# Kernel tuning notes

Measured on AMD Instinct MI355X. Metric: run time of the kernel, lower is better.

Reference implementation:

```python
import jax, jax.numpy as jnp
import numpy as np

B, C, H, W = 256, 1024, 14, 14
C8 = C // 8
TXT = 150 * 1024  # flattened text embed dim
N = H * W  # 196, matches self.l shape (1,196)


def setup_inputs() -> dict:
    key = jax.random.key(0)
    ks = jax.random.split(key, 12)
    s = lambda fan_in: 1.0 / np.sqrt(fan_in)
    return {
        "x": jax.random.normal(ks[0], (B, C, H, W), jnp.float32),
        "text_embed": jax.random.normal(ks[1], (B, 1, 150, 1024), jnp.float32),
        "G_w": jax.random.normal(ks[2], (C, TXT), jnp.float32) * s(TXT),
        "G_b": jnp.zeros((C,), jnp.float32),
        "l": jax.random.normal(ks[3], (1, N), jnp.float32) * 0.02,
        "W_q": jax.random.normal(ks[4], (C8, C), jnp.float32) * s(C),
        "b_q": jnp.zeros((C8,), jnp.float32),
        "W_k": jax.random.normal(ks[5], (C8, C), jnp.float32) * s(C),
        "b_k": jnp.zeros((C8,), jnp.float32),
        "W_v": jax.random.normal(ks[6], (C, C), jnp.float32) * s(C),
        "b_v": jnp.zeros((C,), jnp.float32),
        "gamma": jnp.ones((1,), jnp.float32) * 0.5,
    }


def reference(x, text_embed, G_w, G_b, l, W_q, b_q, W_k, b_k, W_v, b_v, gamma):
    b, c, h, w = x.shape
    n = h * w
    # text preprocessing: squeeze(1) + flatten + Linear G -> (B, C)
    te = text_embed.reshape(b, -1) @ G_w.T + G_b  # (B, C)
    # bmm(te[:, :, None], l broadcast) == outer product per batch -> (B, C, N)
    te_flat = te[:, :, None] * l[None, 0, None, :]  # (B, C, N)
    x_flat = x.reshape(b, c, n)  # (B, C, N)
    # 1x1 convs == channel matmuls
    proj_query = jnp.einsum('qc,bcn->bnq', W_q, x_flat) + b_q  # (B, N, C8)
    proj_key = jnp.einsum('kc,bcn->bkn', W_k, te_flat) + b_k[None, :, None]  # (B, C8, N)
    energy = jnp.einsum('bnq,bqm->bnm', proj_query, proj_key)  # (B, N, N)
    attention = jax.nn.softmax(energy, axis=-1)  # (B, N, N)
    proj_value = jnp.einsum('vc,bcn->bvn', W_v, te_flat) + b_v[None, :, None]  # (B, C, N)
    # out = bmm(value, attention^T): out[b,c,m] = sum_n value[b,c,n] * attn[b,m,n]
    out = jnp.einsum('bcn,bmn->bcm', proj_value, attention)  # (B, C, N)
    out = out.reshape(b, c, h, w)
    return gamma * out + x
```

## Files before the change

kernel.cpp:

```cpp
#include <hip/hip_runtime.h>
#include <hip/hip_bf16.h>

#define BB 256
#define CC 1024
#define CQ 128
#define NN 196
#define TXTK 153600
#define SPLITS 64
#define KCHUNK 2400
#define KSTEPS 75
#define LDP 40

typedef __attribute__((ext_vector_type(8))) short short8;
typedef __attribute__((ext_vector_type(4))) float f32x4;
typedef __attribute__((ext_vector_type(2))) unsigned int u32x2;

static __device__ __forceinline__ unsigned int pkbf(float a, float b) {
  __hip_bfloat162 t = __float22bfloat162_rn(make_float2(a, b));
  unsigned int r;
  __builtin_memcpy(&r, &t, 4);
  return r;
}

static __device__ __forceinline__ float bflo(unsigned int u) {
  unsigned int v = u << 16;
  float f;
  __builtin_memcpy(&f, &v, 4);
  return f;
}
static __device__ __forceinline__ float bfhi(unsigned int u) {
  unsigned int v = u & 0xffff0000u;
  float f;
  __builtin_memcpy(&f, &v, 4);
  return f;
}

__global__ __launch_bounds__(1024) void k1_gemm_partial(
    const float* __restrict__ TE, const float* __restrict__ Gw,
    unsigned int* __restrict__ part) {
  __shared__ unsigned short Al[2][256 * LDP];
  __shared__ unsigned short Bl[2][256 * LDP];

  const int tid = threadIdx.x;
  const int fid = blockIdx.x;
  const int r8 = fid & 7;
  const int nt = (fid >> 3) & 3;
  const int sp = (fid >> 5) * 8 + r8;
  const int kbase = sp * KCHUNK;

  const int lane = tid & 63;
  const int w = tid >> 6;
  const int wm = w & 3;
  const int wn = w >> 2;

  const int r0 = tid >> 3;
  const int c0 = (tid & 7) * 4;
  const float* Ap0 = TE + (size_t)r0 * TXTK + kbase + c0;
  const float* Ap1 = TE + (size_t)(r0 + 128) * TXTK + kbase + c0;
  const float* Bp0 = Gw + (size_t)(nt * 256 + r0) * TXTK + kbase + c0;
  const float* Bp1 = Gw + (size_t)(nt * 256 + r0 + 128) * TXTK + kbase + c0;
  const int l0 = r0 * LDP + c0;
  const int l1 = (r0 + 128) * LDP + c0;

  f32x4 ra0, ra1, rb0, rb1;
  auto loadRegs = [&](int ko) {
    ra0 = *(const f32x4*)(Ap0 + ko);
    ra1 = *(const f32x4*)(Ap1 + ko);
    rb0 = __builtin_nontemporal_load((const f32x4*)(Bp0 + ko));
    rb1 = __builtin_nontemporal_load((const f32x4*)(Bp1 + ko));
  };
  auto cvt4 = [](f32x4 v) {
    uint2 h;
    h.x = pkbf(v.x, v.y);
    h.y = pkbf(v.z, v.w);
    return h;
  };
  auto writeLDS = [&](int buf) {
    *(uint2*)&Al[buf][l0] = cvt4(ra0);
    *(uint2*)&Al[buf][l1] = cvt4(ra1);
    *(uint2*)&Bl[buf][l0] = cvt4(rb0);
    *(uint2*)&Bl[buf][l1] = cvt4(rb1);
  };

  f32x4 acc[4][4];
  const f32x4 z = {0.f, 0.f, 0.f, 0.f};
#pragma unroll
  for (int i = 0; i < 4; ++i)
#pragma unroll
    for (int j = 0; j < 4; ++j) acc[i][j] = z;

  loadRegs(0);
  writeLDS(0);
  __syncthreads();

  const int k8 = (lane >> 4) * 8;
  const int fr = lane & 15;

  for (int ks = 0; ks < KSTEPS; ++ks) {
    const int cur = ks & 1;
    if (ks + 1 < KSTEPS) loadRegs((ks + 1) * 32);

    short8 bfr[4];
#pragma unroll
    for (int ns = 0; ns < 4; ++ns) {
      int col = wn * 64 + ns * 16 + fr;
      bfr[ns] = *(const short8*)&Bl[cur][col * LDP + k8];
    }
#pragma unroll
    for (int ms = 0; ms < 4; ++ms) {
      int row = wm * 64 + ms * 16 + fr;
      short8 af = *(const short8*)&Al[cur][row * LDP + k8];
#pragma unroll
      for (int ns = 0; ns < 4; ++ns)
        acc[ms][ns] = __builtin_amdgcn_mfma_f32_16x16x32_bf16(af, bfr[ns], acc[ms][ns], 0, 0, 0);
    }

    if (ks + 1 < KSTEPS) writeLDS(cur ^ 1);
    __syncthreads();
  }

  u32x2* d2 = (u32x2*)part + (size_t)(sp * 4 + nt) * 16384;
#pragma unroll
  for (int ms = 0; ms < 4; ++ms)
#pragma unroll
    for (int ns = 0; ns < 4; ++ns) {
      u32x2 pk;
      pk.x = pkbf(acc[ms][ns][0], acc[ms][ns][1]);
      pk.y = pkbf(acc[ms][ns][2], acc[ms][ns][3]);
      const int v = ms * 4 + ns;
      __builtin_nontemporal_store(pk, d2 + v * 1024 + tid);
    }
}

__global__ __launch_bounds__(1024) void k2_reduce(
    const unsigned int* __restrict__ part, const float* __restrict__ Gb,
    float* __restrict__ te) {
  const int idx = blockIdx.x * 1024 + threadIdx.x;
  const int nt = idx >> 14;
  const int s = idx & 16383;
  const u32x2* p2 = (const u32x2*)part;

  float a0 = 0.f, a1 = 0.f, a2 = 0.f, a3 = 0.f;
#pragma unroll 4
  for (int sp = 0; sp < SPLITS; ++sp) {
    u32x2 u = p2[(size_t)(sp * 4 + nt) * 16384 + s];
    a0 += bflo(u.x); a1 += bfhi(u.x);
    a2 += bflo(u.y); a3 += bfhi(u.y);
  }

  const int v = s >> 10, t = s & 1023;
  const int lane = t & 63, w = t >> 6;
  const int wm = w & 3, wn = w >> 2;
  const int ms = v >> 2, ns = v & 3;
  const int b0 = wm * 64 + ms * 16 + (lane >> 4) * 4;
  const int c = nt * 256 + wn * 64 + ns * 16 + (lane & 15);
  const float gb = Gb[c];
  te[(size_t)(b0 + 0) * CC + c] = a0 + gb;
  te[(size_t)(b0 + 1) * CC + c] = a1 + gb;
  te[(size_t)(b0 + 2) * CC + c] = a2 + gb;
  te[(size_t)(b0 + 3) * CC + c] = a3 + gb;
}

__global__ __launch_bounds__(256) void k3_dual(
    const float* __restrict__ te, const float* __restrict__ Wk,
    const float* __restrict__ Wv, float* __restrict__ kbuf,
    float* __restrict__ vbuf) {
  __shared__ float As[64][33];
  __shared__ float Bs[64][33];
  const int tid = threadIdx.x;
  const int tx = tid & 15, ty = tid >> 4;
  const int bx = blockIdx.x;
  const float* Wt;
  float* outp;
  int Nout, n0;
  if (bx < 2) { Wt = Wk; outp = kbuf; Nout = CQ; n0 = bx * 64; }
  else        { Wt = Wv; outp = vbuf; Nout = CC; n0 = (bx - 2) * 64; }
  const int m0 = blockIdx.y * 64;
  float acc[4][4] = {};
  for (int k0 = 0; k0 < CC; k0 += 32) {
#pragma unroll
    for (int j = 0; j < 2; ++j) {
      int i = tid + 256 * j;
      int r = i >> 3, c4 = (i & 7) * 4;
      f32x4 va = *(const f32x4*)(te + (size_t)(m0 + r) * CC + k0 + c4);
      As[r][c4 + 0] = va.x; As[r][c4 + 1] = va.y; As[r][c4 + 2] = va.z; As[r][c4 + 3] = va.w;
      f32x4 vb4 = *(const f32x4*)(Wt + (size_t)(n0 + r) * CC + k0 + c4);
      Bs[r][c4 + 0] = vb4.x; Bs[r][c4 + 1] = vb4.y; Bs[r][c4 + 2] = vb4.z; Bs[r][c4 + 3] = vb4.w;
    }
    __syncthreads();
#pragma unroll 8
    for (int k = 0; k < 32; ++k) {
      float a[4], bv[4];
#pragma unroll
      for (int i = 0; i < 4; ++i) a[i] = As[ty * 4 + i][k];
#pragma unroll
      for (int j = 0; j < 4; ++j) bv[j] = Bs[tx * 4 + j][k];
#pragma unroll
      for (int i = 0; i < 4; ++i)
#pragma unroll
        for (int j = 0; j < 4; ++j) acc[i][j] += a[i] * bv[j];
    }
    __syncthreads();
  }
#pragma unroll
  for (int i = 0; i < 4; ++i)
#pragma unroll
    for (int j = 0; j < 4; ++j)
      outp[(size_t)(m0 + ty * 4 + i) * Nout + n0 + tx * 4 + j] = acc[i][j];
}

__global__ __launch_bounds__(1024) void k4a_attn(
    const float* __restrict__ x, const float* __restrict__ kb,
    const float* __restrict__ Wq, const float* __restrict__ bq,
    float* __restrict__ pbuf) {
  __shared__ float kbs[CQ];
  __shared__ float wqs[512];
  __shared__ float partl[16][NN];
  __shared__ float dsh;

  const int h = blockIdx.x;
  const int b = blockIdx.y;
  const int ch0 = h * 512;
  const int tid = threadIdx.x;

  if (tid < CQ) kbs[tid] = kb[b * CQ + tid];
  __syncthreads();

  if (tid < 512) {
    float s = 0.f;
#pragma unroll 8
    for (int q = 0; q < CQ; ++q) s += Wq[q * CC + ch0 + tid] * kbs[q];
    wqs[tid] = s;
  }
  if (tid == 1023) {
    float d = 0.f;
    if (h == 0)
      for (int q = 0; q < CQ; ++q) d += bq[q] * kbs[q];
    dsh = d;
  }
  __syncthreads();

  const float* xb = x + (size_t)b * (CC * NN) + (size_t)ch0 * NN;
  if (tid < 784) {
    const int r = tid / 49, n4 = tid % 49;
    f32x4 acc = {0.f, 0.f, 0.f, 0.f};
#pragma unroll 4
    for (int c = r; c < 512; c += 16) {
      f32x4 v = *(const f32x4*)(xb + c * NN + n4 * 4);
      acc += wqs[c] * v;
    }
    partl[r][n4 * 4 + 0] = acc.x;
    partl[r][n4 * 4 + 1] = acc.y;
    partl[r][n4 * 4 + 2] = acc.z;
    partl[r][n4 * 4 + 3] = acc.w;
  }
  __syncthreads();
  if (tid < NN) {
    float s = dsh;
#pragma unroll
    for (int r = 0; r < 16; ++r) s += partl[r][tid];
    pbuf[b * 400 + h * 200 + tid] = s;
  }
}

__global__ __launch_bounds__(256) void k4mid(
    const float* __restrict__ pbuf, const float* __restrict__ l,
    float* __restrict__ sbuf) {
  __shared__ float ls[NN];
  __shared__ float av[NN];
  const int b = blockIdx.x;
  const int tid = threadIdx.x;
  if (tid < NN) {
    ls[tid] = l[tid];
    av[tid] = pbuf[b * 400 + tid] + pbuf[b * 400 + 200 + tid];
  }
  __syncthreads();
  if (tid < NN) {
    const float a = av[tid];
    float m = -1e30f;
    for (int j = 0; j < NN; ++j) m = fmaxf(m, a * ls[j]);
    float num = 0.f, den = 0.f;
    for (int j = 0; j < NN; ++j) {
      float e = __expf(a * ls[j] - m);
      num += ls[j] * e;
      den += e;
    }
    sbuf[b * NN + tid] = num / den;
  }
}

__global__ __launch_bounds__(256) void k4b_epilogue(
    const float* __restrict__ x, const float* __restrict__ vbuf,
    const float* __restrict__ bv, const float* __restrict__ sbuf,
    const float* __restrict__ gammap, float* __restrict__ out) {
  __shared__ __align__(16) float sv[NN];
  __shared__ float Ac[128];
  __shared__ float Bc[128];
  const int sl = blockIdx.x;
  const int b = blockIdx.y;
  const int tid = threadIdx.x;
  const float g = gammap[0];

  if (tid < NN) sv[tid] = sbuf[b * NN + tid];
  if (tid < 128) {
    Ac[tid] = g * vbuf[b * CC + sl * 128 + tid];
    Bc[tid] = g * bv[sl * 128 + tid];
  }
  __syncthreads();

  const float* xb = x + (size_t)b * (CC * NN) + (size_t)sl * 128 * NN;
  float* ob = out + (size_t)b * (CC * NN) + (size_t)sl * 128 * NN;
  for (int f = tid; f < 6272; f += 256) {
    const int c = f / 49;
    const int n4 = f - c * 49;
    f32x4 xv = *(const f32x4*)(xb + f * 4);
    f32x4 s4 = *(const f32x4*)&sv[n4 * 4];
    f32x4 o = Ac[c] * s4 + (Bc[c] + xv);
    __builtin_nontemporal_store(o, (f32x4*)(ob + f * 4));
  }
}

extern "C" void kernel_launch(void* const* d_in, const int* in_sizes, int n_in,
                              void* d_out, int out_size, void* d_ws, size_t ws_size,
                              hipStream_t stream) {
  const float* x    = (const float*)d_in[0];
  const float* TE   = (const float*)d_in[1];
  const float* Gw   = (const float*)d_in[2];
  const float* Gb   = (const float*)d_in[3];
  const float* l    = (const float*)d_in[4];
  const float* Wq   = (const float*)d_in[5];
  const float* bq   = (const float*)d_in[6];
  const float* Wk   = (const float*)d_in[7];
  const float* Wv   = (const float*)d_in[9];
  const float* bv   = (const float*)d_in[10];
  const float* gam  = (const float*)d_in[11];

  float* out  = (float*)d_out;
  unsigned int* part = (unsigned int*)d_out;
  float* pbuf = out + 20000000;
  float* te   = (float*)d_ws;
  float* kbuf = te + BB * CC;
  float* vbuf = kbuf + BB * CQ;
  float* sbuf = vbuf + BB * CC;

  hipLaunchKernelGGL(k1_gemm_partial, dim3(256), dim3(1024), 0, stream, TE, Gw, part);
  hipLaunchKernelGGL(k2_reduce, dim3(64), dim3(1024), 0, stream, part, Gb, te);
  hipLaunchKernelGGL(k3_dual, dim3(18, 4), dim3(256), 0, stream, te, Wk, Wv, kbuf, vbuf);
  hipLaunchKernelGGL(k4a_attn, dim3(2, BB), dim3(1024), 0, stream, x, kbuf, Wq, bq, pbuf);
  hipLaunchKernelGGL(k4mid, dim3(BB), dim3(256), 0, stream, pbuf, l, sbuf);
  hipLaunchKernelGGL(k4b_epilogue, dim3(8, BB), dim3(256), 0, stream, x, vbuf, bv, sbuf, gam, out);
}
```

Before: 388.7 us.

## Pre-convert text embeddings to tiled bf16 before split-K GEMM

Adds a pre-pass kernel that converts the fp32 text embedding into bf16, stored in the exact per-split, per-step tile order the GEMM consumes. Previously each of the four column-tile blocks read and converted the same fp32 A data. Now A is read once in fp32 and the GEMM streams half-size, contiguous bf16 tiles straight into LDS. Other edits add nontemporal loads in the reduction, reverse batch order in the epilogue, and move pbuf into the workspace. This costs an extra launch and scratch space in the output buffer.

Result: slower. 448.9 us (+15.5%).

```diff
diff --git a/kernel.cpp b/kernel.cpp
--- a/kernel.cpp
+++ b/kernel.cpp
@@ -35,8 +35,26 @@
   return f;
 }
 
+__global__ __launch_bounds__(256) void k0_cvtA(
+    const float* __restrict__ TE, unsigned short* __restrict__ tz) {
+  const int o = blockIdx.x * 256 + threadIdx.x;
+  const int col8 = (o & 3) * 8;
+  const int row = (o >> 2) & 255;
+  const int st = o >> 10;
+  const int sp = st / 75, step = st - sp * 75;
+  const float* src = TE + (size_t)row * TXTK + sp * KCHUNK + step * 32 + col8;
+  f32x4 v0 = __builtin_nontemporal_load((const f32x4*)src);
+  f32x4 v1 = __builtin_nontemporal_load((const f32x4*)(src + 4));
+  uint4 pk;
+  pk.x = pkbf(v0.x, v0.y);
+  pk.y = pkbf(v0.z, v0.w);
+  pk.z = pkbf(v1.x, v1.y);
+  pk.w = pkbf(v1.z, v1.w);
+  *(uint4*)(tz + (size_t)o * 8) = pk;
+}
+
 __global__ __launch_bounds__(1024) void k1_gemm_partial(
-    const float* __restrict__ TE, const float* __restrict__ Gw,
+    const unsigned short* __restrict__ tz, const float* __restrict__ Gw,
     unsigned int* __restrict__ part) {
   __shared__ unsigned short Al[2][256 * LDP];
   __shared__ unsigned short Bl[2][256 * LDP];
@@ -53,19 +71,23 @@
   const int wm = w & 3;
   const int wn = w >> 2;
 
+  const short8* Asrc = (const short8*)tz + (size_t)sp * 75 * 1024 + tid;
+  const int arow = tid >> 2;
+  const int acol = (tid & 3) * 8;
+  const int la = arow * LDP + acol;
+
   const int r0 = tid >> 3;
   const int c0 = (tid & 7) * 4;
-  const float* Ap0 = TE + (size_t)r0 * TXTK + kbase + c0;
-  const float* Ap1 = TE + (size_t)(r0 + 128) * TXTK + kbase + c0;
   const float* Bp0 = Gw + (size_t)(nt * 256 + r0) * TXTK + kbase + c0;
   const float* Bp1 = Gw + (size_t)(nt * 256 + r0 + 128) * TXTK + kbase + c0;
   const int l0 = r0 * LDP + c0;
   const int l1 = (r0 + 128) * LDP + c0;
 
-  f32x4 ra0, ra1, rb0, rb1;
-  auto loadRegs = [&](int ko) {
-    ra0 = *(const f32x4*)(Ap0 + ko);
-    ra1 = *(const f32x4*)(Ap1 + ko);
+  short8 a8;
+  f32x4 rb0, rb1;
+  auto loadRegs = [&](int ks) {
+    a8 = __builtin_nontemporal_load(Asrc + ks * 1024);
+    const int ko = ks * 32;
     rb0 = __builtin_nontemporal_load((const f32x4*)(Bp0 + ko));
     rb1 = __builtin_nontemporal_load((const f32x4*)(Bp1 + ko));
   };
@@ -76,8 +98,7 @@
     return h;
   };
   auto writeLDS = [&](int buf) {
-    *(uint2*)&Al[buf][l0] = cvt4(ra0);
-    *(uint2*)&Al[buf][l1] = cvt4(ra1);
+    *(short8*)&Al[buf][la] = a8;
     *(uint2*)&Bl[buf][l0] = cvt4(rb0);
     *(uint2*)&Bl[buf][l1] = cvt4(rb1);
   };
@@ -98,7 +119,7 @@
 
   for (int ks = 0; ks < KSTEPS; ++ks) {
     const int cur = ks & 1;
-    if (ks + 1 < KSTEPS) loadRegs((ks + 1) * 32);
+    if (ks + 1 < KSTEPS) loadRegs(ks + 1);
 
     short8 bfr[4];
 #pragma unroll
@@ -143,7 +164,7 @@
   float a0 = 0.f, a1 = 0.f, a2 = 0.f, a3 = 0.f;
 #pragma unroll 4
   for (int sp = 0; sp < SPLITS; ++sp) {
-    u32x2 u = p2[(size_t)(sp * 4 + nt) * 16384 + s];
+    u32x2 u = __builtin_nontemporal_load(p2 + (size_t)(sp * 4 + nt) * 16384 + s);
     a0 += bflo(u.x); a1 += bfhi(u.x);
     a2 += bflo(u.y); a3 += bfhi(u.y);
   }
@@ -297,7 +318,7 @@
   __shared__ float Ac[128];
   __shared__ float Bc[128];
   const int sl = blockIdx.x;
-  const int b = blockIdx.y;
+  const int b = 255 - blockIdx.y;
   const int tid = threadIdx.x;
   const float g = gammap[0];
 
@@ -337,13 +358,15 @@
 
   float* out  = (float*)d_out;
   unsigned int* part = (unsigned int*)d_out;
-  float* pbuf = out + 20000000;
+  unsigned short* tz = (unsigned short*)d_out + 16777216;
   float* te   = (float*)d_ws;
   float* kbuf = te + BB * CC;
   float* vbuf = kbuf + BB * CQ;
   float* sbuf = vbuf + BB * CC;
-
-  hipLaunchKernelGGL(k1_gemm_partial, dim3(256), dim3(1024), 0, stream, TE, Gw, part);
+  float* pbuf = sbuf + BB * NN;
+
+  hipLaunchKernelGGL(k0_cvtA, dim3(19200), dim3(256), 0, stream, TE, tz);
+  hipLaunchKernelGGL(k1_gemm_partial, dim3(256), dim3(1024), 0, stream, tz, Gw, part);
   hipLaunchKernelGGL(k2_reduce, dim3(64), dim3(1024), 0, stream, part, Gb, te);
   hipLaunchKernelGGL(k3_dual, dim3(18, 4), dim3(256), 0, stream, te, Wk, Wv, kbuf, vbuf);
   hipLaunchKernelGGL(k4a_attn, dim3(2, BB), dim3(1024), 0, stream, x, kbuf, Wq, bq, pbuf);
```

## Widen split-K GEMM tiles to two N-tiles per block to reuse A loads

Applied to the files above, without the earlier changes.

Each k1 block now computes two 256-column N tiles of the text-embedding GEMM, sharing the A (text_embed) tile in LDS. The K dimension is cut into more, shorter chunks (120 splits of 1280), and the grid shrinks to 240 blocks. This halves redundant reads of the activation matrix and roughly fills the CUs once. In exchange it uses more LDS and doubles the accumulator registers, which may hurt occupancy. It also adds more partials for k2 to reduce, makes k2 loads nontemporal, and moves the pbuf scratch into the workspace.

Result: slower. 1.043 ms (+168.4%).

```diff
diff --git a/kernel.cpp b/kernel.cpp
--- a/kernel.cpp
+++ b/kernel.cpp
@@ -6,9 +6,9 @@
 #define CQ 128
 #define NN 196
 #define TXTK 153600
-#define SPLITS 64
-#define KCHUNK 2400
-#define KSTEPS 75
+#define SPLITS 120
+#define KCHUNK 1280
+#define KSTEPS 40
 #define LDP 40
 
 typedef __attribute__((ext_vector_type(8))) short short8;
@@ -39,13 +39,14 @@
     const float* __restrict__ TE, const float* __restrict__ Gw,
     unsigned int* __restrict__ part) {
   __shared__ unsigned short Al[2][256 * LDP];
-  __shared__ unsigned short Bl[2][256 * LDP];
+  __shared__ unsigned short Bl0[2][256 * LDP];
+  __shared__ unsigned short Bl1[2][256 * LDP];
 
   const int tid = threadIdx.x;
   const int fid = blockIdx.x;
   const int r8 = fid & 7;
-  const int nt = (fid >> 3) & 3;
-  const int sp = (fid >> 5) * 8 + r8;
+  const int p = (fid >> 3) & 1;
+  const int sp = (fid >> 4) * 8 + r8;
   const int kbase = sp * KCHUNK;
 
   const int lane = tid & 63;
@@ -57,17 +58,21 @@
   const int c0 = (tid & 7) * 4;
   const float* Ap0 = TE + (size_t)r0 * TXTK + kbase + c0;
   const float* Ap1 = TE + (size_t)(r0 + 128) * TXTK + kbase + c0;
-  const float* Bp0 = Gw + (size_t)(nt * 256 + r0) * TXTK + kbase + c0;
-  const float* Bp1 = Gw + (size_t)(nt * 256 + r0 + 128) * TXTK + kbase + c0;
+  const float* B0p0 = Gw + (size_t)((p * 2 + 0) * 256 + r0) * TXTK + kbase + c0;
+  const float* B0p1 = B0p0 + (size_t)128 * TXTK;
+  const float* B1p0 = Gw + (size_t)((p * 2 + 1) * 256 + r0) * TXTK + kbase + c0;
+  const float* B1p1 = B1p0 + (size_t)128 * TXTK;
   const int l0 = r0 * LDP + c0;
   const int l1 = (r0 + 128) * LDP + c0;
 
-  f32x4 ra0, ra1, rb0, rb1;
+  f32x4 ra0, ra1, rb00, rb01, rb10, rb11;
   auto loadRegs = [&](int ko) {
     ra0 = *(const f32x4*)(Ap0 + ko);
     ra1 = *(const f32x4*)(Ap1 + ko);
-    rb0 = __builtin_nontemporal_load((const f32x4*)(Bp0 + ko));
-    rb1 = __builtin_nontemporal_load((const f32x4*)(Bp1 + ko));
+    rb00 = __builtin_nontemporal_load((const f32x4*)(B0p0 + ko));
+    rb01 = __builtin_nontemporal_load((const f32x4*)(B0p1 + ko));
+    rb10 = __builtin_nontemporal_load((const f32x4*)(B1p0 + ko));
+    rb11 = __builtin_nontemporal_load((const f32x4*)(B1p1 + ko));
   };
   auto cvt4 = [](f32x4 v) {
     uint2 h;
@@ -78,16 +83,18 @@
   auto writeLDS = [&](int buf) {
     *(uint2*)&Al[buf][l0] = cvt4(ra0);
     *(uint2*)&Al[buf][l1] = cvt4(ra1);
-    *(uint2*)&Bl[buf][l0] = cvt4(rb0);
-    *(uint2*)&Bl[buf][l1] = cvt4(rb1);
+    *(uint2*)&Bl0[buf][l0] = cvt4(rb00);
+    *(uint2*)&Bl0[buf][l1] = cvt4(rb01);
+    *(uint2*)&Bl1[buf][l0] = cvt4(rb10);
+    *(uint2*)&Bl1[buf][l1] = cvt4(rb11);
   };
 
-  f32x4 acc[4][4];
+  f32x4 acc0[4][4], acc1[4][4];
   const f32x4 z = {0.f, 0.f, 0.f, 0.f};
 #pragma unroll
   for (int i = 0; i < 4; ++i)
 #pragma unroll
-    for (int j = 0; j < 4; ++j) acc[i][j] = z;
+    for (int j = 0; j < 4; ++j) { acc0[i][j] = z; acc1[i][j] = z; }
 
   loadRegs(0);
   writeLDS(0);
@@ -100,11 +107,12 @@
     const int cur = ks & 1;
     if (ks + 1 < KSTEPS) loadRegs((ks + 1) * 32);
 
-    short8 bfr[4];
+    short8 bfr0[4], bfr1[4];
 #pragma unroll
     for (int ns = 0; ns < 4; ++ns) {
       int col = wn * 64 + ns * 16 + fr;
-      bfr[ns] = *(const short8*)&Bl[cur][col * LDP + k8];
+      bfr0[ns] = *(const short8*)&Bl0[cur][col * LDP + k8];
+      bfr1[ns] = *(const short8*)&Bl1[cur][col * LDP + k8];
     }
 #pragma unroll
     for (int ms = 0; ms < 4; ++ms) {
@@ -112,23 +120,30 @@
       short8 af = *(const short8*)&Al[cur][row * LDP + k8];
 #pragma unroll
       for (int ns = 0; ns < 4; ++ns)
-        acc[ms][ns] = __builtin_amdgcn_mfma_f32_16x16x32_bf16(af, bfr[ns], acc[ms][ns], 0, 0, 0);
+        acc0[ms][ns] = __builtin_amdgcn_mfma_f32_16x16x32_bf16(af, bfr0[ns], acc0[ms][ns], 0, 0, 0);
+#pragma unroll
+      for (int ns = 0; ns < 4; ++ns)
+        acc1[ms][ns] = __builtin_amdgcn_mfma_f32_16x16x32_bf16(af, bfr1[ns], acc1[ms][ns], 0, 0, 0);
     }
 
     if (ks + 1 < KSTEPS) writeLDS(cur ^ 1);
     __syncthreads();
   }
 
-  u32x2* d2 = (u32x2*)part + (size_t)(sp * 4 + nt) * 16384;
+  u32x2* d20 = (u32x2*)part + (size_t)(sp * 4 + p * 2 + 0) * 16384;
+  u32x2* d21 = (u32x2*)part + (size_t)(sp * 4 + p * 2 + 1) * 16384;
 #pragma unroll
   for (int ms = 0; ms < 4; ++ms)
 #pragma unroll
     for (int ns = 0; ns < 4; ++ns) {
+      const int v = ms * 4 + ns;
       u32x2 pk;
-      pk.x = pkbf(acc[ms][ns][0], acc[ms][ns][1]);
-      pk.y = pkbf(acc[ms][ns][2], acc[ms][ns][3]);
-      const int v = ms * 4 + ns;
-      __builtin_nontemporal_store(pk, d2 + v * 1024 + tid);
+      pk.x = pkbf(acc0[ms][ns][0], acc0[ms][ns][1]);
+      pk.y = pkbf(acc0[ms][ns][2], acc0[ms][ns][3]);
+      __builtin_nontemporal_store(pk, d20 + v * 1024 + tid);
+      pk.x = pkbf(acc1[ms][ns][0], acc1[ms][ns][1]);
+      pk.y = pkbf(acc1[ms][ns][2], acc1[ms][ns][3]);
+      __builtin_nontemporal_store(pk, d21 + v * 1024 + tid);
     }
 }
 
@@ -143,7 +158,7 @@
   float a0 = 0.f, a1 = 0.f, a2 = 0.f, a3 = 0.f;
 #pragma unroll 4
   for (int sp = 0; sp < SPLITS; ++sp) {
-    u32x2 u = p2[(size_t)(sp * 4 + nt) * 16384 + s];
+    u32x2 u = __builtin_nontemporal_load(p2 + (size_t)(sp * 4 + nt) * 16384 + s);
     a0 += bflo(u.x); a1 += bfhi(u.x);
     a2 += bflo(u.y); a3 += bfhi(u.y);
   }
@@ -337,13 +352,13 @@
 
   float* out  = (float*)d_out;
   unsigned int* part = (unsigned int*)d_out;
-  float* pbuf = out + 20000000;
   float* te   = (float*)d_ws;
   float* kbuf = te + BB * CC;
   float* vbuf = kbuf + BB * CQ;
   float* sbuf = vbuf + BB * CC;
-
-  hipLaunchKernelGGL(k1_gemm_partial, dim3(256), dim3(1024), 0, stream, TE, Gw, part);
+  float* pbuf = sbuf + BB * NN;
+
+  hipLaunchKernelGGL(k1_gemm_partial, dim3(240), dim3(1024), 0, stream, TE, Gw, part);
   hipLaunchKernelGGL(k2_reduce, dim3(64), dim3(1024), 0, stream, part, Gb, te);
   hipLaunchKernelGGL(k3_dual, dim3(18, 4), dim3(256), 0, stream, te, Wk, Wv, kbuf, vbuf);
   hipLaunchKernelGGL(k4a_attn, dim3(2, BB), dim3(1024), 0, stream, x, kbuf, Wq, bq, pbuf);
```

## Split K1 GEMM tiles into 128x256 blocks of 512 threads

Applied to the files above, without the earlier changes.

The split-K text GEMM now uses 512 blocks of 512 threads. Each block computes a 128-row by 256-column tile instead of 256x256, with block ordering changed so the split index varies fastest. The aim is higher occupancy and more resident blocks per CU for this memory-bound GEMM. The cost is that the G_w weights are read twice, once per M half, which adds global traffic. The reduce kernel and partial layout are updated to match, reduce loads become nontemporal, and pbuf moves from the output buffer into workspace.

Result: slower. 432.0 us (+11.1%).

```diff
diff --git a/kernel.cpp b/kernel.cpp
--- a/kernel.cpp
+++ b/kernel.cpp
@@ -35,39 +35,46 @@
   return f;
 }
 
-__global__ __launch_bounds__(1024) void k1_gemm_partial(
+__global__ __launch_bounds__(512, 4) void k1_gemm_partial(
     const float* __restrict__ TE, const float* __restrict__ Gw,
     unsigned int* __restrict__ part) {
-  __shared__ unsigned short Al[2][256 * LDP];
+  __shared__ unsigned short Al[2][128 * LDP];
   __shared__ unsigned short Bl[2][256 * LDP];
 
   const int tid = threadIdx.x;
   const int fid = blockIdx.x;
-  const int r8 = fid & 7;
-  const int nt = (fid >> 3) & 3;
-  const int sp = (fid >> 5) * 8 + r8;
+  const int sp = fid & 63;
+  const int mnt = fid >> 6;
+  const int m = mnt >> 2;
+  const int nt = mnt & 3;
   const int kbase = sp * KCHUNK;
 
   const int lane = tid & 63;
   const int w = tid >> 6;
-  const int wm = w & 3;
-  const int wn = w >> 2;
+  const int wm = w & 1;
+  const int wn = w >> 1;
 
   const int r0 = tid >> 3;
   const int c0 = (tid & 7) * 4;
-  const float* Ap0 = TE + (size_t)r0 * TXTK + kbase + c0;
-  const float* Ap1 = TE + (size_t)(r0 + 128) * TXTK + kbase + c0;
+  const float* Ap0 = TE + (size_t)(m * 128 + r0) * TXTK + kbase + c0;
+  const float* Ap1 = Ap0 + (size_t)64 * TXTK;
   const float* Bp0 = Gw + (size_t)(nt * 256 + r0) * TXTK + kbase + c0;
-  const float* Bp1 = Gw + (size_t)(nt * 256 + r0 + 128) * TXTK + kbase + c0;
+  const float* Bp1 = Bp0 + (size_t)64 * TXTK;
+  const float* Bp2 = Bp0 + (size_t)128 * TXTK;
+  const float* Bp3 = Bp0 + (size_t)192 * TXTK;
   const int l0 = r0 * LDP + c0;
-  const int l1 = (r0 + 128) * LDP + c0;
-
-  f32x4 ra0, ra1, rb0, rb1;
+  const int l1 = (r0 + 64) * LDP + c0;
+  const int l2 = (r0 + 128) * LDP + c0;
+  const int l3 = (r0 + 192) * LDP + c0;
+
+  f32x4 ra0, ra1, rb0, rb1, rb2, rb3;
   auto loadRegs = [&](int ko) {
     ra0 = *(const f32x4*)(Ap0 + ko);
     ra1 = *(const f32x4*)(Ap1 + ko);
     rb0 = __builtin_nontemporal_load((const f32x4*)(Bp0 + ko));
     rb1 = __builtin_nontemporal_load((const f32x4*)(Bp1 + ko));
+    rb2 = __builtin_nontemporal_load((const f32x4*)(Bp2 + ko));
+    rb3 = __builtin_nontemporal_load((const f32x4*)(Bp3 + ko));
   };
   auto cvt4 = [](f32x4 v) {
     uint2 h;
@@ -80,6 +87,8 @@
     *(uint2*)&Al[buf][l1] = cvt4(ra1);
     *(uint2*)&Bl[buf][l0] = cvt4(rb0);
     *(uint2*)&Bl[buf][l1] = cvt4(rb1);
+    *(uint2*)&Bl[buf][l2] = cvt4(rb2);
+    *(uint2*)&Bl[buf][l3] = cvt4(rb3);
   };
 
   f32x4 acc[4][4];
@@ -119,7 +128,7 @@
     __syncthreads();
   }
 
-  u32x2* d2 = (u32x2*)part + (size_t)(sp * 4 + nt) * 16384;
+  u32x2* d2 = (u32x2*)part + (size_t)fid * 8192;
 #pragma unroll
   for (int ms = 0; ms < 4; ++ms)
 #pragma unroll
@@ -128,7 +137,7 @@
       pk.x = pkbf(acc[ms][ns][0], acc[ms][ns][1]);
       pk.y = pkbf(acc[ms][ns][2], acc[ms][ns][3]);
       const int v = ms * 4 + ns;
-      __builtin_nontemporal_store(pk, d2 + v * 1024 + tid);
+      __builtin_nontemporal_store(pk, d2 + v * 512 + tid);
     }
 }
 
@@ -136,23 +145,24 @@
     const unsigned int* __restrict__ part, const float* __restrict__ Gb,
     float* __restrict__ te) {
   const int idx = blockIdx.x * 1024 + threadIdx.x;
-  const int nt = idx >> 14;
-  const int s = idx & 16383;
+  const int mnt = idx >> 13;
+  const int s = idx & 8191;
   const u32x2* p2 = (const u32x2*)part;
 
   float a0 = 0.f, a1 = 0.f, a2 = 0.f, a3 = 0.f;
 #pragma unroll 4
   for (int sp = 0; sp < SPLITS; ++sp) {
-    u32x2 u = p2[(size_t)(sp * 4 + nt) * 16384 + s];
+    u32x2 u = __builtin_nontemporal_load(p2 + (size_t)(mnt * 64 + sp) * 8192 + s);
     a0 += bflo(u.x); a1 += bfhi(u.x);
     a2 += bflo(u.y); a3 += bfhi(u.y);
   }
 
-  const int v = s >> 10, t = s & 1023;
+  const int v = s >> 9, t = s & 511;
   const int lane = t & 63, w = t >> 6;
-  const int wm = w & 3, wn = w >> 2;
+  const int wm = w & 1, wn = w >> 1;
   const int ms = v >> 2, ns = v & 3;
-  const int b0 = wm * 64 + ms * 16 + (lane >> 4) * 4;
+  const int m = mnt >> 2, nt = mnt & 3;
+  const int b0 = m * 128 + wm * 64 + ms * 16 + (lane >> 4) * 4;
   const int c = nt * 256 + wn * 64 + ns * 16 + (lane & 15);
   const float gb = Gb[c];
   te[(size_t)(b0 + 0) * CC + c] = a0 + gb;
@@ -337,13 +347,13 @@
 
   float* out  = (float*)d_out;
   unsigned int* part = (unsigned int*)d_out;
-  float* pbuf = out + 20000000;
   float* te   = (float*)d_ws;
   float* kbuf = te + BB * CC;
   float* vbuf = kbuf + BB * CQ;
   float* sbuf = vbuf + BB * CC;
-
-  hipLaunchKernelGGL(k1_gemm_partial, dim3(256), dim3(1024), 0, stream, TE, Gw, part);
+  float* pbuf = sbuf + BB * NN;
+
+  hipLaunchKernelGGL(k1_gemm_partial, dim3(512), dim3(512), 0, stream, TE, Gw, part);
   hipLaunchKernelGGL(k2_reduce, dim3(64), dim3(1024), 0, stream, part, Gb, te);
   hipLaunchKernelGGL(k3_dual, dim3(18, 4), dim3(256), 0, stream, te, Wk, Wv, kbuf, vbuf);
   hipLaunchKernelGGL(k4a_attn, dim3(2, BB), dim3(1024), 0, stream, x, kbuf, Wq, bq, pbuf);
```
